# Optimization experiments

Measured on AMD Instinct MI355X. Metric: run time of the kernel, lower is better.

The kernel has to match this reference:

```python
import math
import jax, jax.numpy as jnp
import numpy as np

NUM_BUCKETS = 32
MAX_DISTANCE = 128
B, T, E, H, D = 2, 2048, 1024, 16, 64
INIT_SCALE = 0.1


def _relative_position_bucket(rel, num_buckets=NUM_BUCKETS, max_distance=MAX_DISTANCE):
    # T5-style bucketing; rel is int [T, T]
    nb = num_buckets // 2
    buckets = (rel > 0).astype(jnp.int32) * nb
    rel_abs = jnp.abs(rel)
    max_exact = nb // 2
    is_small = rel_abs < max_exact
    # guard log(0); those positions are selected by is_small anyway
    val_large = max_exact + (
        jnp.log(jnp.maximum(rel_abs, 1).astype(jnp.float32) / max_exact)
        / math.log(max_distance / max_exact) * (nb - max_exact)
    ).astype(jnp.int32)
    val_large = jnp.minimum(val_large, nb - 1)
    return buckets + jnp.where(is_small, rel_abs, val_large)


def setup_inputs() -> dict:
    key = jax.random.key(0)
    ks = jax.random.split(key, 6)
    x = jax.random.normal(ks[0], (B, T, E), dtype=jnp.float32)
    # nn.Linear weights are [out_features, in_features], init normal(std=0.1)
    Wq = jax.random.normal(ks[1], (H * D, E), dtype=jnp.float32) * INIT_SCALE
    Wk = jax.random.normal(ks[2], (H * D, E), dtype=jnp.float32) * INIT_SCALE
    Wv = jax.random.normal(ks[3], (H * D, E), dtype=jnp.float32) * INIT_SCALE
    Wo = jax.random.normal(ks[4], (E, H * D), dtype=jnp.float32) * INIT_SCALE
    # nn.Embedding default init: standard normal
    rel_emb = jax.random.normal(ks[5], (NUM_BUCKETS, H), dtype=jnp.float32)
    return {"x": x, "Wq": Wq, "Wk": Wk, "Wv": Wv, "Wo": Wo, "rel_emb": rel_emb}


def reference(x, Wq, Wk, Wv, Wo, rel_emb):
    b, t, _ = x.shape
    scale = D ** (-0.5)
    q = jnp.einsum('bte,fe->btf', x, Wq).reshape(b, t, H, D).transpose(0, 2, 1, 3)
    k = jnp.einsum('bte,fe->btf', x, Wk).reshape(b, t, H, D).transpose(0, 2, 1, 3)
    v = jnp.einsum('bte,fe->btf', x, Wv).reshape(b, t, H, D).transpose(0, 2, 1, 3)
    attn = jnp.einsum('bhtd,bhsd->bhts', q, k) * scale  # [B,H,T,T]
    # T5 relative position bias
    pos = jnp.arange(t)
    rel = pos[:, None] - pos[None, :]
    buckets = _relative_position_bucket(rel)
    bias = rel_emb[buckets]                    # [T,T,H]
    attn = attn + bias.transpose(2, 0, 1)[None]  # [1,H,T,T]
    # causal mask (triu, diagonal=1)
    causal = jnp.triu(jnp.ones((t, t), dtype=bool), k=1)
    attn = jnp.where(causal[None, None], -jnp.inf, attn)
    attn = jax.nn.softmax(attn, axis=-1)
    out = jnp.einsum('bhts,bhsd->bhtd', attn, v).transpose(0, 2, 1, 3).reshape(b, t, H * D)
    return jnp.einsum('btf,ef->bte', out, Wo)
```

## Files before the change

### kernel.cpp

```cpp
#include <hip/hip_runtime.h>
#include <hip/hip_bf16.h>
#include <stdint.h>


typedef __attribute__((ext_vector_type(8))) short bf16x8;
typedef __attribute__((ext_vector_type(4))) float f32x4;

#define MFMA16(a, b, c) __builtin_amdgcn_mfma_f32_16x16x32_bf16((a), (b), (c), 0, 0, 0)

typedef __attribute__((address_space(1))) void gvoid_t;
typedef __attribute__((address_space(3))) void lvoid_t;

__device__ __forceinline__ void gload16(const void* g, void* l) {
    __builtin_amdgcn_global_load_lds((gvoid_t*)g, (lvoid_t*)l, 16, 0, 0);
}

__device__ __forceinline__ ushort f2bf_rne(float f) {
    union { float f; uint32_t u; } v; v.f = f;
    uint32_t u = v.u;
    return (ushort)((u + 0x7FFFu + ((u >> 16) & 1u)) >> 16);
}

__global__ void cvt_all(const float* __restrict__ x,
                        const float* __restrict__ wq, const float* __restrict__ wk,
                        const float* __restrict__ wv, const float* __restrict__ wo,
                        ushort* __restrict__ out) {
    int i = (blockIdx.x * 256 + threadIdx.x) * 4;
    int sel = i >> 20;
    const float* src; int off;
    if (sel < 4) { src = x; off = i; }
    else {
        src = (sel == 4) ? wq : (sel == 5) ? wk : (sel == 6) ? wv : wo;
        off = i & 1048575;
    }
    float4 f = *(const float4*)(src + off);
    ushort4 o;
    o.x = f2bf_rne(f.x); o.y = f2bf_rne(f.y);
    o.z = f2bf_rne(f.z); o.w = f2bf_rne(f.w);
    *(ushort4*)(out + i) = o;
}

__global__ void build_bias(const float* __restrict__ rel_emb, float* __restrict__ bias_tab) {
    int idx = blockIdx.x * 256 + threadIdx.x;
    int h = idx >> 11, rel = idx & 2047;
    int bucket;
    if (rel == 0) bucket = 0;
    else if (rel < 8) bucket = 16 + rel;
    else {
        int t;
        if      (rel >= 91) t = 7;
        else if (rel >= 64) t = 6;
        else if (rel >= 46) t = 5;
        else if (rel >= 32) t = 4;
        else if (rel >= 23) t = 3;
        else if (rel >= 16) t = 2;
        else if (rel >= 12) t = 1;
        else                t = 0;
        bucket = 24 + t;
    }
    bias_tab[idx] = rel_emb[bucket * 16 + h];
}

template<int MODE>
__global__ __launch_bounds__(256, MODE == 0 ? 3 : 4) void gemm_bt(
    const ushort* __restrict__ A,
    const ushort* __restrict__ W0, const ushort* __restrict__ W1, const ushort* __restrict__ W2,
    ushort* __restrict__ outq, ushort* __restrict__ outk, ushort* __restrict__ outvt,
    float* __restrict__ outf)
{
    constexpr int BM  = (MODE == 0) ? 128 : 64;
    constexpr int ACH = BM / 64;
    constexpr int MI  = (MODE == 0) ? 4 : 2;
    __shared__ __align__(16) ushort lsA[2][BM * 32];
    __shared__ __align__(16) ushort lsB[2][128 * 32];
    const int tid = threadIdx.x;
    const int lane = tid & 63, w = tid >> 6;
    const int g = lane >> 4, c16 = lane & 15;
    const int m0 = blockIdx.x * BM;
    const int wm = w >> 1, wn = w & 1;

    const ushort* W;
    int n0, widx = 0;
    if (MODE == 0) {
        widx = blockIdx.y >> 3;
        W = (widx == 0) ? W0 : (widx == 1) ? W1 : W2;
        n0 = (blockIdx.y & 7) * 128;
    } else {
        W = W0;
        n0 = blockIdx.y * 128;
    }

    f32x4 acc[MI][4];
    #pragma unroll
    for (int i = 0; i < MI; i++)
        #pragma unroll
        for (int j = 0; j < 4; j++) acc[i][j] = (f32x4){0.f, 0.f, 0.f, 0.f};

    int acrow[ACH], acj[ACH], bcrow[2], bcj[2];
    #pragma unroll
    for (int i = 0; i < ACH; i++) {
        int c = (i * 4 + w) * 64 + lane;
        acrow[i] = c >> 2; acj[i] = (c & 3) ^ ((acrow[i] >> 1) & 3);
    }
    #pragma unroll
    for (int i = 0; i < 2; i++) {
        int c = (i * 4 + w) * 64 + lane;
        bcrow[i] = c >> 2; bcj[i] = (c & 3) ^ ((bcrow[i] >> 1) & 3);
    }

    auto stage = [&](int buf, int kt) {
        #pragma unroll
        for (int i = 0; i < ACH; i++)
            gload16(A + (size_t)(m0 + acrow[i]) * 1024 + kt + acj[i] * 8,
                    &lsA[buf][(i * 4 + w) * 512]);
        #pragma unroll
        for (int i = 0; i < 2; i++)
            gload16(W + (size_t)(n0 + bcrow[i]) * 1024 + kt + bcj[i] * 8,
                    &lsB[buf][(i * 4 + w) * 512]);
    };

    stage(0, 0);
    __syncthreads();

    for (int it = 0; it < 32; ++it) {
        const int cur = it & 1;
        if (it < 31) stage(cur ^ 1, (it + 1) * 32);
        bf16x8 af[MI], bfv[4];
        #pragma unroll
        for (int mi = 0; mi < MI; mi++) {
            int row = wm * (16 * MI) + mi * 16 + c16;
            af[mi] = *(const bf16x8*)(&lsA[cur][row * 32 + ((g ^ ((row >> 1) & 3)) * 8)]);
        }
        #pragma unroll
        for (int ni = 0; ni < 4; ni++) {
            int row = wn * 64 + ni * 16 + c16;
            bfv[ni] = *(const bf16x8*)(&lsB[cur][row * 32 + ((g ^ ((row >> 1) & 3)) * 8)]);
        }
        #pragma unroll
        for (int mi = 0; mi < MI; mi++)
            #pragma unroll
            for (int ni = 0; ni < 4; ni++)
                acc[mi][ni] = MFMA16(af[mi], bfv[ni], acc[mi][ni]);
        __syncthreads();
    }

    const float qs = (MODE == 0 && 0 == (blockIdx.y >> 3)) ? 0.125f : 1.0f;
    #pragma unroll
    for (int mi = 0; mi < MI; mi++) {
        #pragma unroll
        for (int ni = 0; ni < 4; ni++) {
            int mg = m0 + wm * (16 * MI) + mi * 16 + g * 4;
            if (MODE == 0) {
                int f = n0 + wn * 64 + ni * 16 + c16;
                int h = f >> 6, d = f & 63;
                if (widx < 2) {
                    ushort* dst = (widx == 0) ? outq : outk;
                    #pragma unroll
                    for (int r = 0; r < 4; r++) {
                        int m = mg + r, b = m >> 11, t = m & 2047;
                        dst[((b * 16 + h) * 2048 + t) * 64 + d] = f2bf_rne(acc[mi][ni][r] * qs);
                    }
                } else {
                    int b = mg >> 11, t = mg & 2047;
                    ushort4 pk;
                    pk.x = f2bf_rne(acc[mi][ni][0]); pk.y = f2bf_rne(acc[mi][ni][1]);
                    pk.z = f2bf_rne(acc[mi][ni][2]); pk.w = f2bf_rne(acc[mi][ni][3]);
                    *(ushort4*)(outvt + ((size_t)(b * 16 + h) * 64 + d) * 2048 + t) = pk;
                }
            } else {
                int ng = n0 + wn * 64 + ni * 16 + c16;
                #pragma unroll
                for (int r = 0; r < 4; r++) {
                    int m = mg + r;
                    outf[(size_t)m * 1024 + ng] = acc[mi][ni][r];
                }
            }
        }
    }
}

__global__ __launch_bounds__(256, 4) void attn_kernel(
    const ushort* __restrict__ qb_, const ushort* __restrict__ kb_,
    const ushort* __restrict__ vtb, const float* __restrict__ bias_tab,
    ushort* __restrict__ ob)
{
    __shared__ __align__(16) ushort Ks[64 * 64];
    __shared__ __align__(16) ushort Vs[64 * 64];
    __shared__ __align__(16) ushort Ps[4][16 * 72];

    const int tid = threadIdx.x, lane = tid & 63, w = tid >> 6;
    const int g = lane >> 4, c16 = lane & 15;
    const int bh = blockIdx.y;
    const int qb = (blockIdx.x + bh) & 31;
    const int b = bh >> 4, h = bh & 15;

    const ushort* qh = qb_ + (size_t)bh * 2048 * 64;
    const ushort* kh = kb_ + (size_t)bh * 2048 * 64;
    const ushort* vh = vtb + (size_t)bh * 64 * 2048;
    const float* bt = bias_tab + h * 2048;
    const int q0 = qb * 64;

    int crow[2], cj[2];
    #pragma unroll
    for (int i = 0; i < 2; i++) {
        int c = (i * 4 + w) * 64 + lane;
        crow[i] = c >> 3;
        cj[i] = (c & 7) ^ (crow[i] & 7);
    }

    const int qrow = q0 + w * 16 + c16;
    bf16x8 qf[2];
    #pragma unroll
    for (int kk = 0; kk < 2; kk++)
        qf[kk] = *(const bf16x8*)(qh + (size_t)qrow * 64 + kk * 32 + g * 8);

    float m_run = -1e30f, l_run = 0.f;
    f32x4 o[4];
    #pragma unroll
    for (int ni = 0; ni < 4; ni++) o[ni] = (f32x4){0.f, 0.f, 0.f, 0.f};
    const float bias_far = bt[128];

    for (int j64 = 0; j64 <= qb; j64++) {
        const int k0 = j64 * 64;
        __syncthreads();
        #pragma unroll
        for (int i = 0; i < 2; i++) {
            gload16(kh + (size_t)(k0 + crow[i]) * 64 + cj[i] * 8, Ks + (i * 4 + w) * 512);
            gload16(vh + (size_t)crow[i] * 2048 + k0 + cj[i] * 8, Vs + (i * 4 + w) * 512);
        }
        __syncthreads();

        f32x4 s[4];
        #pragma unroll
        for (int f = 0; f < 4; f++) s[f] = (f32x4){0.f, 0.f, 0.f, 0.f};
        __builtin_amdgcn_s_setprio(1);
        #pragma unroll
        for (int kk = 0; kk < 2; kk++) {
            #pragma unroll
            for (int f = 0; f < 4; f++) {
                int row = f * 16 + c16;
                bf16x8 a = *(const bf16x8*)(Ks + row * 64 + (((kk * 4 + g) ^ (row & 7)) * 8));
                s[f] = MFMA16(a, qf[kk], s[f]);
            }
        }
        __builtin_amdgcn_s_setprio(0);

        const bool near = (qb - j64) < 3;
        const bool diag = (j64 == qb);
        float p[4][4];
        float m_new, lt = 0.f;
        if (near) {
            float mt = -1e30f;
            #pragma unroll
            for (int f = 0; f < 4; f++)
                #pragma unroll
                for (int r = 0; r < 4; r++) {
                    int kpos = k0 + f * 16 + g * 4 + r;
                    int rel = qrow - kpos;
                    float lg;
                    if (diag && rel < 0) lg = -1e30f;
                    else lg = s[f][r] + bt[rel];
                    p[f][r] = lg;
                    mt = fmaxf(mt, lg);
                }
            mt = fmaxf(mt, __shfl_xor(mt, 16));
            mt = fmaxf(mt, __shfl_xor(mt, 32));
            m_new = fmaxf(m_run, mt);
            #pragma unroll
            for (int f = 0; f < 4; f++)
                #pragma unroll
                for (int r = 0; r < 4; r++) {
                    float e = __expf(p[f][r] - m_new);
                    p[f][r] = e;
                    lt += e;
                }
        } else {
            float mt = -1e30f;
            #pragma unroll
            for (int f = 0; f < 4; f++)
                #pragma unroll
                for (int r = 0; r < 4; r++) mt = fmaxf(mt, s[f][r]);
            mt = fmaxf(mt, __shfl_xor(mt, 16));
            mt = fmaxf(mt, __shfl_xor(mt, 32));
            m_new = fmaxf(m_run, mt + bias_far);
            float madj = m_new - bias_far;
            #pragma unroll
            for (int f = 0; f < 4; f++)
                #pragma unroll
                for (int r = 0; r < 4; r++) {
                    float e = __expf(s[f][r] - madj);
                    p[f][r] = e;
                    lt += e;
                }
        }
        lt += __shfl_xor(lt, 16);
        lt += __shfl_xor(lt, 32);
        float alpha = __expf(m_run - m_new);
        l_run = l_run * alpha + lt;
        m_run = m_new;
        #pragma unroll
        for (int ni = 0; ni < 4; ni++) {
            o[ni][0] *= alpha; o[ni][1] *= alpha; o[ni][2] *= alpha; o[ni][3] *= alpha;
        }

        #pragma unroll
        for (int f = 0; f < 4; f++) {
            ushort4 pk;
            pk.x = f2bf_rne(p[f][0]); pk.y = f2bf_rne(p[f][1]);
            pk.z = f2bf_rne(p[f][2]); pk.w = f2bf_rne(p[f][3]);
            *(ushort4*)(&Ps[w][c16 * 72 + f * 16 + g * 4]) = pk;
        }
        __builtin_amdgcn_s_setprio(1);
        #pragma unroll
        for (int kk = 0; kk < 2; kk++) {
            bf16x8 pf = *(const bf16x8*)(&Ps[w][c16 * 72 + kk * 32 + g * 8]);
            #pragma unroll
            for (int ni = 0; ni < 4; ni++) {
                int row = ni * 16 + c16;
                bf16x8 av = *(const bf16x8*)(Vs + row * 64 + (((kk * 4 + g) ^ (row & 7)) * 8));
                o[ni] = MFMA16(av, pf, o[ni]);
            }
        }
        __builtin_amdgcn_s_setprio(0);
    }

    float inv = 1.f / l_run;
    size_t base = ((size_t)(b * 2048 + qrow)) * 1024 + h * 64;
    #pragma unroll
    for (int ni = 0; ni < 4; ni++) {
        ushort4 pk;
        pk.x = f2bf_rne(o[ni][0] * inv); pk.y = f2bf_rne(o[ni][1] * inv);
        pk.z = f2bf_rne(o[ni][2] * inv); pk.w = f2bf_rne(o[ni][3] * inv);
        *(ushort4*)(ob + base + ni * 16 + g * 4) = pk;
    }
}

extern "C" void kernel_launch(void* const* d_in, const int* in_sizes, int n_in,
                              void* d_out, int out_size, void* d_ws, size_t ws_size,
                              hipStream_t stream) {
    const float* x       = (const float*)d_in[0];
    const float* Wq      = (const float*)d_in[1];
    const float* Wk      = (const float*)d_in[2];
    const float* Wv      = (const float*)d_in[3];
    const float* Wo      = (const float*)d_in[4];
    const float* rel_emb = (const float*)d_in[5];

    char* ws = (char*)d_ws;
    ushort* xbf = (ushort*)(ws);
    ushort* wqb = (ushort*)(ws + (8u  << 20));
    ushort* wkb = (ushort*)(ws + (10u << 20));
    ushort* wvb = (ushort*)(ws + (12u << 20));
    ushort* wob = (ushort*)(ws + (14u << 20));
    ushort* qbf = (ushort*)(ws + (16u << 20));
    ushort* kbf = (ushort*)(ws + (24u << 20));
    ushort* vtb = (ushort*)(ws + (32u << 20));
    ushort* obf = (ushort*)(ws + (40u << 20));
    float*  btab = (float*)(ws + (48u << 20));

    cvt_all<<<8192, 256, 0, stream>>>(x, Wq, Wk, Wv, Wo, xbf);
    build_bias<<<128, 256, 0, stream>>>(rel_emb, btab);

    gemm_bt<0><<<dim3(32, 24), 256, 0, stream>>>(xbf, wqb, wkb, wvb, qbf, kbf, vtb, nullptr);
    attn_kernel<<<dim3(32, 32), 256, 0, stream>>>(qbf, kbf, vtb, btab, obf);
    gemm_bt<1><<<dim3(64, 8), 256, 0, stream>>>(obf, wob, nullptr, nullptr,
                                                nullptr, nullptr, nullptr, (float*)d_out);
}
```

Before: 190.5 us.

## Pair causal query blocks per attention CTA and use single-buffered 64-wide GEMM K tiles

The attention kernel now launches half as many blocks, and each block processes query block px and then 31-px in turn, so every CTA does the same amount of causal work. This replaces the earlier rotated single-block mapping, which left CTAs with very uneven loads. The GEMM drops its double-buffered 32-wide K staging in favour of a single 64-wide K tile with two syncs per iteration, and changes the MODE 1 occupancy hint. That halves the number of loop iterations but gives up the overlap of loads with MFMA work, and the attention grid shrinks to 512 CTAs, which may underfill the GPU.

```diff
diff --git a/kernel.cpp b/kernel.cpp
--- a/kernel.cpp
+++ b/kernel.cpp
@@ -62,17 +62,17 @@
 }
 
 template<int MODE>
-__global__ __launch_bounds__(256, MODE == 0 ? 3 : 4) void gemm_bt(
+__global__ __launch_bounds__(256, MODE == 0 ? 3 : 2) void gemm_bt(
     const ushort* __restrict__ A,
     const ushort* __restrict__ W0, const ushort* __restrict__ W1, const ushort* __restrict__ W2,
     ushort* __restrict__ outq, ushort* __restrict__ outk, ushort* __restrict__ outvt,
     float* __restrict__ outf)
 {
     constexpr int BM  = (MODE == 0) ? 128 : 64;
-    constexpr int ACH = BM / 64;
+    constexpr int ACH = BM / 32;
     constexpr int MI  = (MODE == 0) ? 4 : 2;
-    __shared__ __align__(16) ushort lsA[2][BM * 32];
-    __shared__ __align__(16) ushort lsB[2][128 * 32];
+    __shared__ __align__(16) ushort lsA[BM * 64];
+    __shared__ __align__(16) ushort lsB[128 * 64];
     const int tid = threadIdx.x;
     const int lane = tid & 63, w = tid >> 6;
     const int g = lane >> 4, c16 = lane & 15;
@@ -96,55 +96,51 @@
         #pragma unroll
         for (int j = 0; j < 4; j++) acc[i][j] = (f32x4){0.f, 0.f, 0.f, 0.f};
 
-    int acrow[ACH], acj[ACH], bcrow[2], bcj[2];
+    int acrow[ACH], acj[ACH], bcrow[4], bcj[4];
     #pragma unroll
     for (int i = 0; i < ACH; i++) {
         int c = (i * 4 + w) * 64 + lane;
-        acrow[i] = c >> 2; acj[i] = (c & 3) ^ ((acrow[i] >> 1) & 3);
-    }
-    #pragma unroll
-    for (int i = 0; i < 2; i++) {
+        acrow[i] = c >> 3; acj[i] = (c & 7) ^ (acrow[i] & 7);
+    }
+    #pragma unroll
+    for (int i = 0; i < 4; i++) {
         int c = (i * 4 + w) * 64 + lane;
-        bcrow[i] = c >> 2; bcj[i] = (c & 3) ^ ((bcrow[i] >> 1) & 3);
-    }
-
-    auto stage = [&](int buf, int kt) {
+        bcrow[i] = c >> 3; bcj[i] = (c & 7) ^ (bcrow[i] & 7);
+    }
+
+    for (int kt = 0; kt < 1024; kt += 64) {
+        __syncthreads();
         #pragma unroll
         for (int i = 0; i < ACH; i++)
             gload16(A + (size_t)(m0 + acrow[i]) * 1024 + kt + acj[i] * 8,
-                    &lsA[buf][(i * 4 + w) * 512]);
-        #pragma unroll
-        for (int i = 0; i < 2; i++)
+                    lsA + (i * 4 + w) * 512);
+        #pragma unroll
+        for (int i = 0; i < 4; i++)
             gload16(W + (size_t)(n0 + bcrow[i]) * 1024 + kt + bcj[i] * 8,
-                    &lsB[buf][(i * 4 + w) * 512]);
-    };
-
-    stage(0, 0);
-    __syncthreads();
-
-    for (int it = 0; it < 32; ++it) {
-        const int cur = it & 1;
-        if (it < 31) stage(cur ^ 1, (it + 1) * 32);
-        bf16x8 af[MI], bfv[4];
-        #pragma unroll
-        for (int mi = 0; mi < MI; mi++) {
-            int row = wm * (16 * MI) + mi * 16 + c16;
-            af[mi] = *(const bf16x8*)(&lsA[cur][row * 32 + ((g ^ ((row >> 1) & 3)) * 8)]);
+                    lsB + (i * 4 + w) * 512);
+        __syncthreads();
+        #pragma unroll
+        for (int kk = 0; kk < 2; kk++) {
+            bf16x8 af[MI], bfv[4];
+            #pragma unroll
+            for (int mi = 0; mi < MI; mi++) {
+                int row = wm * (16 * MI) + mi * 16 + c16;
+                af[mi] = *(const bf16x8*)(lsA + row * 64 + (((kk * 4 + g) ^ (row & 7)) * 8));
+            }
+            #pragma unroll
+            for (int ni = 0; ni < 4; ni++) {
+                int row = wn * 64 + ni * 16 + c16;
+                bfv[ni] = *(const bf16x8*)(lsB + row * 64 + (((kk * 4 + g) ^ (row & 7)) * 8));
+            }
+            #pragma unroll
+            for (int mi = 0; mi < MI; mi++)
+                #pragma unroll
+                for (int ni = 0; ni < 4; ni++)
+                    acc[mi][ni] = MFMA16(af[mi], bfv[ni], acc[mi][ni]);
         }
-        #pragma unroll
-        for (int ni = 0; ni < 4; ni++) {
-            int row = wn * 64 + ni * 16 + c16;
-            bfv[ni] = *(const bf16x8*)(&lsB[cur][row * 32 + ((g ^ ((row >> 1) & 3)) * 8)]);
-        }
-        #pragma unroll
-        for (int mi = 0; mi < MI; mi++)
-            #pragma unroll
-            for (int ni = 0; ni < 4; ni++)
-                acc[mi][ni] = MFMA16(af[mi], bfv[ni], acc[mi][ni]);
-        __syncthreads();
-    }
-
-    const float qs = (MODE == 0 && 0 == (blockIdx.y >> 3)) ? 0.125f : 1.0f;
+    }
+
+    const float qs = (MODE == 0 && widx == 0) ? 0.125f : 1.0f;
     #pragma unroll
     for (int mi = 0; mi < MI; mi++) {
         #pragma unroll
@@ -191,14 +187,14 @@
     const int tid = threadIdx.x, lane = tid & 63, w = tid >> 6;
     const int g = lane >> 4, c16 = lane & 15;
     const int bh = blockIdx.y;
-    const int qb = (blockIdx.x + bh) & 31;
+    const int px = blockIdx.x;
     const int b = bh >> 4, h = bh & 15;
 
     const ushort* qh = qb_ + (size_t)bh * 2048 * 64;
     const ushort* kh = kb_ + (size_t)bh * 2048 * 64;
     const ushort* vh = vtb + (size_t)bh * 64 * 2048;
     const float* bt = bias_tab + h * 2048;
-    const int q0 = qb * 64;
+    const float bias_far = bt[128];
 
     int crow[2], cj[2];
     #pragma unroll
@@ -208,130 +204,134 @@
         cj[i] = (c & 7) ^ (crow[i] & 7);
     }
 
-    const int qrow = q0 + w * 16 + c16;
-    bf16x8 qf[2];
-    #pragma unroll
-    for (int kk = 0; kk < 2; kk++)
-        qf[kk] = *(const bf16x8*)(qh + (size_t)qrow * 64 + kk * 32 + g * 8);
-
-    float m_run = -1e30f, l_run = 0.f;
-    f32x4 o[4];
-    #pragma unroll
-    for (int ni = 0; ni < 4; ni++) o[ni] = (f32x4){0.f, 0.f, 0.f, 0.f};
-    const float bias_far = bt[128];
-
-    for (int j64 = 0; j64 <= qb; j64++) {
-        const int k0 = j64 * 64;
-        __syncthreads();
-        #pragma unroll
-        for (int i = 0; i < 2; i++) {
-            gload16(kh + (size_t)(k0 + crow[i]) * 64 + cj[i] * 8, Ks + (i * 4 + w) * 512);
-            gload16(vh + (size_t)crow[i] * 2048 + k0 + cj[i] * 8, Vs + (i * 4 + w) * 512);
+    for (int half = 0; half < 2; half++) {
+        const int qb = half ? 31 - px : px;
+        const int q0 = qb * 64;
+        const int qrow = q0 + w * 16 + c16;
+
+        bf16x8 qf[2];
+        #pragma unroll
+        for (int kk = 0; kk < 2; kk++)
+            qf[kk] = *(const bf16x8*)(qh + (size_t)qrow * 64 + kk * 32 + g * 8);
+
+        float m_run = -1e30f, l_run = 0.f;
+        f32x4 o[4];
+        #pragma unroll
+        for (int ni = 0; ni < 4; ni++) o[ni] = (f32x4){0.f, 0.f, 0.f, 0.f};
+
+        for (int j64 = 0; j64 <= qb; j64++) {
+            const int k0 = j64 * 64;
+            __syncthreads();
+            #pragma unroll
+            for (int i = 0; i < 2; i++) {
+                gload16(kh + (size_t)(k0 + crow[i]) * 64 + cj[i] * 8, Ks + (i * 4 + w) * 512);
+                gload16(vh + (size_t)crow[i] * 2048 + k0 + cj[i] * 8, Vs + (i * 4 + w) * 512);
+            }
+            __syncthreads();
+
+            f32x4 s[4];
+            #pragma unroll
+            for (int f = 0; f < 4; f++) s[f] = (f32x4){0.f, 0.f, 0.f, 0.f};
+            __builtin_amdgcn_s_setprio(1);
+            #pragma unroll
+            for (int kk = 0; kk < 2; kk++) {
+                #pragma unroll
+                for (int f = 0; f < 4; f++) {
+                    int row = f * 16 + c16;
+                    bf16x8 a = *(const bf16x8*)(Ks + row * 64 + (((kk * 4 + g) ^ (row & 7)) * 8));
+                    s[f] = MFMA16(a, qf[kk], s[f]);
+                }
+            }
+            __builtin_amdgcn_s_setprio(0);
+
+            const bool near = (qb - j64) < 3;
+            const bool diag = (j64 == qb);
+            float p[4][4];
+            float m_new, lt = 0.f;
+            if (near) {
+                float mt = -1e30f;
+                #pragma unroll
+                for (int f = 0; f < 4; f++)
+                    #pragma unroll
+                    for (int r = 0; r < 4; r++) {
+                        int kpos = k0 + f * 16 + g * 4 + r;
+                        int rel = qrow - kpos;
+                        float lg;
+                        if (diag && rel < 0) lg = -1e30f;
+                        else lg = s[f][r] + bt[rel];
+                        p[f][r] = lg;
+                        mt = fmaxf(mt, lg);
+                    }
+                mt = fmaxf(mt, __shfl_xor(mt, 16));
+                mt = fmaxf(mt, __shfl_xor(mt, 32));
+                m_new = fmaxf(m_run, mt);
+                #pragma unroll
+                for (int f = 0; f < 4; f++)
+                    #pragma unroll
+                    for (int r = 0; r < 4; r++) {
+                        float e = __expf(p[f][r] - m_new);
+                        p[f][r] = e;
+                        lt += e;
+                    }
+            } else {
+                float mt = -1e30f;
+                #pragma unroll
+                for (int f = 0; f < 4; f++)
+                    #pragma unroll
+                    for (int r = 0; r < 4; r++) mt = fmaxf(mt, s[f][r]);
+                mt = fmaxf(mt, __shfl_xor(mt, 16));
+                mt = fmaxf(mt, __shfl_xor(mt, 32));
+                m_new = fmaxf(m_run, mt + bias_far);
+                float madj = m_new - bias_far;
+                #pragma unroll
+                for (int f = 0; f < 4; f++)
+                    #pragma unroll
+                    for (int r = 0; r < 4; r++) {
+                        float e = __expf(s[f][r] - madj);
+                        p[f][r] = e;
+                        lt += e;
+                    }
+            }
+            lt += __shfl_xor(lt, 16);
+            lt += __shfl_xor(lt, 32);
+            float alpha = __expf(m_run - m_new);
+            l_run = l_run * alpha + lt;
+            m_run = m_new;
+            #pragma unroll
+            for (int ni = 0; ni < 4; ni++) {
+                o[ni][0] *= alpha; o[ni][1] *= alpha; o[ni][2] *= alpha; o[ni][3] *= alpha;
+            }
+
+            #pragma unroll
+            for (int f = 0; f < 4; f++) {
+                ushort4 pk;
+                pk.x = f2bf_rne(p[f][0]); pk.y = f2bf_rne(p[f][1]);
+                pk.z = f2bf_rne(p[f][2]); pk.w = f2bf_rne(p[f][3]);
+                *(ushort4*)(&Ps[w][c16 * 72 + f * 16 + g * 4]) = pk;
+            }
+            __builtin_amdgcn_s_setprio(1);
+            #pragma unroll
+            for (int kk = 0; kk < 2; kk++) {
+                bf16x8 pf = *(const bf16x8*)(&Ps[w][c16 * 72 + kk * 32 + g * 8]);
+                #pragma unroll
+                for (int ni = 0; ni < 4; ni++) {
+                    int row = ni * 16 + c16;
+                    bf16x8 av = *(const bf16x8*)(Vs + row * 64 + (((kk * 4 + g) ^ (row & 7)) * 8));
+                    o[ni] = MFMA16(av, pf, o[ni]);
+                }
+            }
+            __builtin_amdgcn_s_setprio(0);
         }
-        __syncthreads();
-
-        f32x4 s[4];
-        #pragma unroll
-        for (int f = 0; f < 4; f++) s[f] = (f32x4){0.f, 0.f, 0.f, 0.f};
-        __builtin_amdgcn_s_setprio(1);
-        #pragma unroll
-        for (int kk = 0; kk < 2; kk++) {
-            #pragma unroll
-            for (int f = 0; f < 4; f++) {
-                int row = f * 16 + c16;
-                bf16x8 a = *(const bf16x8*)(Ks + row * 64 + (((kk * 4 + g) ^ (row & 7)) * 8));
-                s[f] = MFMA16(a, qf[kk], s[f]);
-            }
+
+        float inv = 1.f / l_run;
+        size_t base = ((size_t)(b * 2048 + qrow)) * 1024 + h * 64;
+        #pragma unroll
+        for (int ni = 0; ni < 4; ni++) {
+            ushort4 pk;
+            pk.x = f2bf_rne(o[ni][0] * inv); pk.y = f2bf_rne(o[ni][1] * inv);
+            pk.z = f2bf_rne(o[ni][2] * inv); pk.w = f2bf_rne(o[ni][3] * inv);
+            *(ushort4*)(ob + base + ni * 16 + g * 4) = pk;
         }
-        __builtin_amdgcn_s_setprio(0);
-
-        const bool near = (qb - j64) < 3;
-        const bool diag = (j64 == qb);
-        float p[4][4];
-        float m_new, lt = 0.f;
-        if (near) {
-            float mt = -1e30f;
-            #pragma unroll
-            for (int f = 0; f < 4; f++)
-                #pragma unroll
-                for (int r = 0; r < 4; r++) {
-                    int kpos = k0 + f * 16 + g * 4 + r;
-                    int rel = qrow - kpos;
-                    float lg;
-                    if (diag && rel < 0) lg = -1e30f;
-                    else lg = s[f][r] + bt[rel];
-                    p[f][r] = lg;
-                    mt = fmaxf(mt, lg);
-                }
-            mt = fmaxf(mt, __shfl_xor(mt, 16));
-            mt = fmaxf(mt, __shfl_xor(mt, 32));
-            m_new = fmaxf(m_run, mt);
-            #pragma unroll
-            for (int f = 0; f < 4; f++)
-                #pragma unroll
-                for (int r = 0; r < 4; r++) {
-                    float e = __expf(p[f][r] - m_new);
-                    p[f][r] = e;
-                    lt += e;
-                }
-        } else {
-            float mt = -1e30f;
-            #pragma unroll
-            for (int f = 0; f < 4; f++)
-                #pragma unroll
-                for (int r = 0; r < 4; r++) mt = fmaxf(mt, s[f][r]);
-            mt = fmaxf(mt, __shfl_xor(mt, 16));
-            mt = fmaxf(mt, __shfl_xor(mt, 32));
-            m_new = fmaxf(m_run, mt + bias_far);
-            float madj = m_new - bias_far;
-            #pragma unroll
-            for (int f = 0; f < 4; f++)
-                #pragma unroll
-                for (int r = 0; r < 4; r++) {
-                    float e = __expf(s[f][r] - madj);
-                    p[f][r] = e;
-                    lt += e;
-                }
-        }
-        lt += __shfl_xor(lt, 16);
-        lt += __shfl_xor(lt, 32);
-        float alpha = __expf(m_run - m_new);
-        l_run = l_run * alpha + lt;
-        m_run = m_new;
-        #pragma unroll
-        for (int ni = 0; ni < 4; ni++) {
-            o[ni][0] *= alpha; o[ni][1] *= alpha; o[ni][2] *= alpha; o[ni][3] *= alpha;
-        }
-
-        #pragma unroll
-        for (int f = 0; f < 4; f++) {
-            ushort4 pk;
-            pk.x = f2bf_rne(p[f][0]); pk.y = f2bf_rne(p[f][1]);
-            pk.z = f2bf_rne(p[f][2]); pk.w = f2bf_rne(p[f][3]);
-            *(ushort4*)(&Ps[w][c16 * 72 + f * 16 + g * 4]) = pk;
-        }
-        __builtin_amdgcn_s_setprio(1);
-        #pragma unroll
-        for (int kk = 0; kk < 2; kk++) {
-            bf16x8 pf = *(const bf16x8*)(&Ps[w][c16 * 72 + kk * 32 + g * 8]);
-            #pragma unroll
-            for (int ni = 0; ni < 4; ni++) {
-                int row = ni * 16 + c16;
-                bf16x8 av = *(const bf16x8*)(Vs + row * 64 + (((kk * 4 + g) ^ (row & 7)) * 8));
-                o[ni] = MFMA16(av, pf, o[ni]);
-            }
-        }
-        __builtin_amdgcn_s_setprio(0);
-    }
-
-    float inv = 1.f / l_run;
-    size_t base = ((size_t)(b * 2048 + qrow)) * 1024 + h * 64;
-    #pragma unroll
-    for (int ni = 0; ni < 4; ni++) {
-        ushort4 pk;
-        pk.x = f2bf_rne(o[ni][0] * inv); pk.y = f2bf_rne(o[ni][1] * inv);
-        pk.z = f2bf_rne(o[ni][2] * inv); pk.w = f2bf_rne(o[ni][3] * inv);
-        *(ushort4*)(ob + base + ni * 16 + g * 4) = pk;
     }
 }
 
@@ -361,7 +361,7 @@
     build_bias<<<128, 256, 0, stream>>>(rel_emb, btab);
 
     gemm_bt<0><<<dim3(32, 24), 256, 0, stream>>>(xbf, wqb, wkb, wvb, qbf, kbf, vtb, nullptr);
-    attn_kernel<<<dim3(32, 32), 256, 0, stream>>>(qbf, kbf, vtb, btab, obf);
+    attn_kernel<<<dim3(16, 32), 256, 0, stream>>>(qbf, kbf, vtb, btab, obf);
     gemm_bt<1><<<dim3(64, 8), 256, 0, stream>>>(obf, wob, nullptr, nullptr,
                                                 nullptr, nullptr, nullptr, (float*)d_out);
 }
```

Measured after the change: 186.1 us. 1.02x faster.
